# Performance work log

Measured on AMD Instinct MI355X. Metric: run time of the kernel, lower is better.

The kernel has to match this reference:

```python
import jax, jax.numpy as jnp
import numpy as np

B, N, V, F, H, O, NCONV = 4096, 64, 100, 128, 256, 1, 4
NEG_SLOPE = 0.01  # torch nn.LeakyReLU default


def leaky(x):
    return jnp.where(x >= 0, x, NEG_SLOPE * x)


def setup_inputs() -> dict:
    key = jax.random.key(0)
    ks = jax.random.split(key, 16)
    node_mat = jax.random.normal(ks[0], (B, N, V), dtype=jnp.float32)
    a = (jax.random.uniform(ks[1], (B, N, N)) < 0.15).astype(jnp.float32)
    adj_mat = jnp.maximum(a, jnp.swapaxes(a, 1, 2))
    s = 0.05
    params = dict(
        W_init=s * jax.random.normal(ks[2], (V, F), jnp.float32),
        b_init=jnp.zeros((F,), jnp.float32),
        W_conv=s * jax.random.normal(ks[3], (NCONV, F, F), jnp.float32),
        b_conv=jnp.zeros((NCONV, F), jnp.float32),
        W_fc0=s * jax.random.normal(ks[4], (F, H), jnp.float32),
        b_fc0=jnp.zeros((H,), jnp.float32),
        W_fc1=s * jax.random.normal(ks[5], (H, H), jnp.float32),
        b_fc1=jnp.zeros((H,), jnp.float32),
        W_out=s * jax.random.normal(ks[6], (H, O), jnp.float32),
        b_out=jnp.zeros((O,), jnp.float32),
    )
    return dict(node_mat=node_mat, adj_mat=adj_mat, **params)


def reference(node_mat, adj_mat, W_init, b_init, W_conv, b_conv,
              W_fc0, b_fc0, W_fc1, b_fc1, W_out, b_out):
    # init transform + LeakyReLU
    x = leaky(node_mat @ W_init + b_init)                      # [B, N, F]
    # degree-normalized adjacency: diag(1/deg) @ A == row-scale (exact same math
    # as the original eye-expand + double bmm, without the NxN diagonal matmul)
    deg = jnp.clip(adj_mat.sum(axis=-1, keepdims=True), 1.0, None)  # [B, N, 1]
    A_norm = adj_mat / deg                                     # [B, N, N]
    for i in range(W_conv.shape[0]):
        agg = jnp.einsum('bij,bjf->bif', A_norm, x)            # neighbor mean
        x = leaky(agg @ W_conv[i] + b_conv[i])
    # mean pooling over atoms
    g = x.mean(axis=1)                                         # [B, F]
    # fc head (dropout p=0 -> identity)
    h = leaky(g @ W_fc0 + b_fc0)
    h = leaky(h @ W_fc1 + b_fc1)
    return h @ W_out + b_out                                   # [B, O]
```

## Files before the change

kernel.cpp:

```cpp
#include <hip/hip_runtime.h>

#define NATOMS 64
#define VDIM 100
#define FDIM 128
#define HDIM 256
#define NCONV 4

typedef __bf16 bf16x8 __attribute__((ext_vector_type(8)));
typedef __bf16 bf16x4 __attribute__((ext_vector_type(4)));
typedef float f32x4 __attribute__((ext_vector_type(4)));

__device__ __forceinline__ float lrelu(float x) {
  return x >= 0.0f ? x : 0.01f * x;
}

__global__ void prep_weights(const float* __restrict__ Wi,
                             const float* __restrict__ Wc,
                             __bf16* __restrict__ WtI,
                             __bf16* __restrict__ WtC) {
  int idx = blockIdx.x * 256 + threadIdx.x;
  int e = idx & 7;
  int lane = (idx >> 3) & 63;
  int ks = (idx >> 9) & 3;
  int n16 = (idx >> 11) & 7;
  int l = idx >> 14;
  int n = n16 * 16 + (lane & 15);
  int k = ks * 32 + (lane >> 4) * 8 + e;
  if (l == 0) {
    WtI[idx] = (__bf16)(k < VDIM ? Wi[k * FDIM + n] : 0.0f);
  } else {
    WtC[(l - 1) * 16384 + (idx & 16383)] =
        (__bf16)Wc[(l - 1) * FDIM * FDIM + k * FDIM + n];
  }
}

template <bool PRODUCE_FRAG>
__device__ __forceinline__ void conv_step(
    const __bf16* __restrict__ Wt, const float* __restrict__ bias,
    const __bf16* __restrict__ sRow, bf16x8 xfrag[2][2], float psum[2],
    const int w, const int lane) {
  const int lr = lane & 15;
  const int g = lane >> 4;
  const int k0 = g * 8;
  f32x4 acc[2][4];
#pragma unroll
  for (int ni = 0; ni < 2; ++ni)
#pragma unroll
    for (int mi = 0; mi < 4; ++mi) acc[ni][mi] = {0.f, 0.f, 0.f, 0.f};
#pragma unroll
  for (int ks = 0; ks < 4; ++ks) {
    bf16x8 bfrag[2], afrag[4];
#pragma unroll
    for (int ni = 0; ni < 2; ++ni)
      bfrag[ni] = *(const bf16x8*)&Wt[(((2 * w + ni) * 4 + ks) * 64 + lane) * 8];
#pragma unroll
    for (int mi = 0; mi < 4; ++mi) {
      int m = mi * 16 + lr;
      afrag[mi] = *(const bf16x8*)&sRow[m * 128 + ((ks * 32 + k0) ^ ((m & 7) << 3))];
    }
#pragma unroll
    for (int ni = 0; ni < 2; ++ni)
#pragma unroll
      for (int mi = 0; mi < 4; ++mi)
        acc[ni][mi] = __builtin_amdgcn_mfma_f32_16x16x32_bf16(
            afrag[mi], bfrag[ni], acc[ni][mi], 0, 0, 0);
  }
#pragma unroll
  for (int ni = 0; ni < 2; ++ni) {
    float bv = bias[(2 * w + ni) * 16 + lr];
    if constexpr (PRODUCE_FRAG) {
      uint2 d[4];
#pragma unroll
      for (int mi = 0; mi < 4; ++mi) {
        bf16x4 o;
#pragma unroll
        for (int j = 0; j < 4; ++j) o[j] = (__bf16)lrelu(acc[ni][mi][j] + bv);
        d[mi] = __builtin_bit_cast(uint2, o);
      }
#pragma unroll
      for (int ksp = 0; ksp < 2; ++ksp) {
        unsigned r[4];
#pragma unroll
        for (int q = 0; q < 4; ++q) {
          int src = (2 * (g & 1) + (q >> 1)) * 16 + lr;
          unsigned lo = (q & 1) ? d[2 * ksp].y : d[2 * ksp].x;
          unsigned hi = (q & 1) ? d[2 * ksp + 1].y : d[2 * ksp + 1].x;
          unsigned va = (unsigned)__shfl((int)lo, src);
          unsigned vb = (unsigned)__shfl((int)hi, src);
          r[q] = (g >> 1) ? vb : va;
        }
        xfrag[ni][ksp] =
            __builtin_bit_cast(bf16x8, make_uint4(r[0], r[1], r[2], r[3]));
      }
    } else {
      float s = 0.f;
#pragma unroll
      for (int mi = 0; mi < 4; ++mi)
#pragma unroll
        for (int j = 0; j < 4; ++j) s += lrelu(acc[ni][mi][j] + bv);
      psum[ni] = s;
    }
  }
}

__device__ __forceinline__ void agg_step(const __bf16* __restrict__ sAdj,
                                         const bf16x8 xfrag[2][2],
                                         __bf16* __restrict__ sRow,
                                         const float rdgv[4], const int w,
                                         const int lane) {
  const int lr = lane & 15;
  const int g = lane >> 4;
  const int k0 = g * 8;
  f32x4 acc[2][4];
#pragma unroll
  for (int mi = 0; mi < 2; ++mi)
#pragma unroll
    for (int ni = 0; ni < 4; ++ni) acc[mi][ni] = {0.f, 0.f, 0.f, 0.f};
#pragma unroll
  for (int ks = 0; ks < 2; ++ks) {
    bf16x8 bfrag[4];
#pragma unroll
    for (int ni = 0; ni < 4; ++ni) {
      int n = ni * 16 + lr;
      bfrag[ni] = *(const bf16x8*)&sAdj[n * 64 + ((ks * 32 + k0) ^ ((n & 7) << 3))];
    }
#pragma unroll
    for (int mi = 0; mi < 2; ++mi)
#pragma unroll
      for (int ni = 0; ni < 4; ++ni)
        acc[mi][ni] = __builtin_amdgcn_mfma_f32_16x16x32_bf16(
            xfrag[mi][ks], bfrag[ni], acc[mi][ni], 0, 0, 0);
  }
#pragma unroll
  for (int ni = 0; ni < 4; ++ni) {
    float rv = rdgv[ni];
    int a = ni * 16 + lr;
#pragma unroll
    for (int mi = 0; mi < 2; ++mi) {
      int f0r = (2 * w + mi) * 16 + g * 4;
      bf16x4 o;
#pragma unroll
      for (int j = 0; j < 4; ++j) o[j] = (__bf16)(acc[mi][ni][j] * rv);
      *(bf16x4*)&sRow[a * 128 + (f0r ^ ((a & 7) << 3))] = o;
    }
  }
}

__launch_bounds__(256, 4)
__global__ void gcn_mfma(const float* __restrict__ node,
                         const float* __restrict__ adj,
                         const __bf16* __restrict__ WtI,
                         const __bf16* __restrict__ WtC,
                         const float* __restrict__ b_init,
                         const float* __restrict__ b_conv,
                         float* __restrict__ g_out) {
  __shared__ __align__(16) __bf16 sRow[NATOMS * FDIM];
  __shared__ __align__(16) __bf16 sAdj[NATOMS * NATOMS];
  __shared__ float sRdg[NATOMS];

  const int b = blockIdx.x;
  const int t = threadIdx.x;
  const int lane = t & 63;
  const int w = t >> 6;

  {
    const float* adjB = adj + (size_t)b * NATOMS * NATOMS;
#pragma unroll
    for (int half = 0; half < 2; ++half) {
      int n = (t >> 3) + half * 32;
      int gi = t & 7;
      float4 a0 = *(const float4*)&adjB[n * 64 + gi * 8];
      float4 a1 = *(const float4*)&adjB[n * 64 + gi * 8 + 4];
      bf16x8 v;
      v[0] = (__bf16)a0.x; v[1] = (__bf16)a0.y; v[2] = (__bf16)a0.z; v[3] = (__bf16)a0.w;
      v[4] = (__bf16)a1.x; v[5] = (__bf16)a1.y; v[6] = (__bf16)a1.z; v[7] = (__bf16)a1.w;
      *(bf16x8*)&sAdj[n * 64 + ((gi * 8) ^ ((n & 7) << 3))] = v;
      float p = a0.x + a0.y + a0.z + a0.w + a1.x + a1.y + a1.z + a1.w;
      p += __shfl_xor(p, 1); p += __shfl_xor(p, 2); p += __shfl_xor(p, 4);
      if (gi == 0) sRdg[n] = 1.0f / fmaxf(p, 1.0f);
    }
  }
  {
    const float* nodeB = node + (size_t)b * NATOMS * VDIM;
#pragma unroll
    for (int u0 = 0; u0 < 4; ++u0) {
      int u = t + 256 * u0;
      int n = u >> 4, gi = u & 15, kk = gi * 8;
      bf16x8 v;
      if (kk + 8 <= VDIM) {
        float4 a0 = *(const float4*)&nodeB[n * VDIM + kk];
        float4 a1 = *(const float4*)&nodeB[n * VDIM + kk + 4];
        v[0] = (__bf16)a0.x; v[1] = (__bf16)a0.y; v[2] = (__bf16)a0.z; v[3] = (__bf16)a0.w;
        v[4] = (__bf16)a1.x; v[5] = (__bf16)a1.y; v[6] = (__bf16)a1.z; v[7] = (__bf16)a1.w;
      } else {
#pragma unroll
        for (int i = 0; i < 8; ++i)
          v[i] = (__bf16)((kk + i < VDIM) ? nodeB[n * VDIM + kk + i] : 0.0f);
      }
      *(bf16x8*)&sRow[n * 128 + (kk ^ ((n & 7) << 3))] = v;
    }
  }
  __syncthreads();

  float rdgv[4];
#pragma unroll
  for (int ni = 0; ni < 4; ++ni) rdgv[ni] = sRdg[ni * 16 + (lane & 15)];

  bf16x8 xfrag[2][2];
  float psum[2];

  conv_step<true>(WtI, b_init, sRow, xfrag, psum, w, lane);
  __syncthreads();

#pragma unroll
  for (int l = 0; l < NCONV; ++l) {
    agg_step(sAdj, xfrag, sRow, rdgv, w, lane);
    __syncthreads();
    if (l < NCONV - 1) {
      conv_step<true>(WtC + l * 16384, b_conv + l * FDIM, sRow, xfrag, psum, w, lane);
      __syncthreads();
    } else {
      conv_step<false>(WtC + l * 16384, b_conv + l * FDIM, sRow, xfrag, psum, w, lane);
    }
  }

#pragma unroll
  for (int ni = 0; ni < 2; ++ni) {
    float s = psum[ni];
    s += __shfl_xor(s, 16);
    s += __shfl_xor(s, 32);
    if (lane < 16)
      g_out[(size_t)b * FDIM + (2 * w + ni) * 16 + lane] = s * (1.0f / 64.0f);
  }
}

__launch_bounds__(256, 2)
__global__ void head_fc(const float* __restrict__ g,
                        const float* __restrict__ W_fc0, const float* __restrict__ b_fc0,
                        const float* __restrict__ W_fc1, const float* __restrict__ b_fc1,
                        const float* __restrict__ W_out, const float* __restrict__ b_out,
                        float* __restrict__ out) {
  __shared__ __align__(16) float sG[16 * FDIM];
  __shared__ float sH[16 * (HDIM + 1)];
  __shared__ float sRed[4 * 16];

  const int t = threadIdx.x;
  const int lane = t & 63;
  const int w = t >> 6;
  const int r0 = blockIdx.x * 16;

  {
    const float4* gs = (const float4*)(g + (size_t)r0 * FDIM);
    float4* gd = (float4*)sG;
#pragma unroll
    for (int u = 0; u < 2; ++u) gd[t + 256 * u] = gs[t + 256 * u];
  }
  __syncthreads();

  float acc[16];
  {
    float bv = b_fc0[t];
#pragma unroll
    for (int r = 0; r < 16; ++r) acc[r] = bv;
    for (int k = 0; k < FDIM; ++k) {
      float wv = W_fc0[k * HDIM + t];
#pragma unroll
      for (int r = 0; r < 16; ++r) acc[r] += sG[r * FDIM + k] * wv;
    }
#pragma unroll
    for (int r = 0; r < 16; ++r) sH[r * (HDIM + 1) + t] = lrelu(acc[r]);
  }
  __syncthreads();

  {
    float bv = b_fc1[t];
#pragma unroll
    for (int r = 0; r < 16; ++r) acc[r] = bv;
    for (int k = 0; k < HDIM; ++k) {
      float wv = W_fc1[k * HDIM + t];
#pragma unroll
      for (int r = 0; r < 16; ++r) acc[r] += sH[r * (HDIM + 1) + k] * wv;
    }
    float wo = W_out[t];
#pragma unroll
    for (int r = 0; r < 16; ++r) acc[r] = lrelu(acc[r]) * wo;
  }
#pragma unroll
  for (int r = 0; r < 16; ++r) {
    float v = acc[r];
    v += __shfl_down(v, 32); v += __shfl_down(v, 16); v += __shfl_down(v, 8);
    v += __shfl_down(v, 4);  v += __shfl_down(v, 2);  v += __shfl_down(v, 1);
    if (lane == 0) sRed[w * 16 + r] = v;
  }
  __syncthreads();
  if (t < 16)
    out[r0 + t] = sRed[t] + sRed[16 + t] + sRed[32 + t] + sRed[48 + t] + b_out[0];
}

extern "C" void kernel_launch(void* const* d_in, const int* in_sizes, int n_in,
                              void* d_out, int out_size, void* d_ws, size_t ws_size,
                              hipStream_t stream) {
  (void)in_sizes; (void)n_in; (void)ws_size; (void)out_size;
  const float* node   = (const float*)d_in[0];
  const float* adj    = (const float*)d_in[1];
  const float* W_init = (const float*)d_in[2];
  const float* b_init = (const float*)d_in[3];
  const float* W_conv = (const float*)d_in[4];
  const float* b_conv = (const float*)d_in[5];
  const float* W_fc0  = (const float*)d_in[6];
  const float* b_fc0  = (const float*)d_in[7];
  const float* W_fc1  = (const float*)d_in[8];
  const float* b_fc1  = (const float*)d_in[9];
  const float* W_out  = (const float*)d_in[10];
  const float* b_out  = (const float*)d_in[11];
  float* out = (float*)d_out;

  __bf16* WtI = (__bf16*)d_ws;
  __bf16* WtC = WtI + 16384;
  float* g = (float*)((char*)d_ws + 160 * 1024);

  prep_weights<<<320, 256, 0, stream>>>(W_init, W_conv, WtI, WtC);
  gcn_mfma<<<4096, 256, 0, stream>>>(node, adj, WtI, WtC, b_init, b_conv, g);
  head_fc<<<256, 256, 0, stream>>>(g, W_fc0, b_fc0, W_fc1, b_fc1, W_out, b_out, out);
}
```

Before: 142.2 us.

## Double-buffer node features in LDS and keep adjacency fragments in registers

Node features now alternate between two LDS buffers across layers. This drops the barrier after each convolution step. The adjacency MFMA B-fragments are loaded from LDS once into registers and reused by all four aggregation steps, and the adjacency staging area is aliased onto the second feature buffer. The cost is more LDS per block (32KB instead of 24KB) and about 32 extra VGPRs, which could add register pressure or spills under the 4-blocks-per-CU launch bound.

Result: slower. 147.5 us (+3.7%).

```diff
diff --git a/kernel.cpp b/kernel.cpp
--- a/kernel.cpp
+++ b/kernel.cpp
@@ -37,7 +37,7 @@
 template <bool PRODUCE_FRAG>
 __device__ __forceinline__ void conv_step(
     const __bf16* __restrict__ Wt, const float* __restrict__ bias,
-    const __bf16* __restrict__ sRow, bf16x8 xfrag[2][2], float psum[2],
+    const __bf16* __restrict__ bufIn, bf16x8 xfrag[2][2], float psum[2],
     const int w, const int lane) {
   const int lr = lane & 15;
   const int g = lane >> 4;
@@ -56,7 +56,7 @@
 #pragma unroll
     for (int mi = 0; mi < 4; ++mi) {
       int m = mi * 16 + lr;
-      afrag[mi] = *(const bf16x8*)&sRow[m * 128 + ((ks * 32 + k0) ^ ((m & 7) << 3))];
+      afrag[mi] = *(const bf16x8*)&bufIn[m * 128 + ((ks * 32 + k0) ^ ((m & 7) << 3))];
     }
 #pragma unroll
     for (int ni = 0; ni < 2; ++ni)
@@ -103,34 +103,26 @@
   }
 }
 
-__device__ __forceinline__ void agg_step(const __bf16* __restrict__ sAdj,
+__device__ __forceinline__ void agg_step(const bf16x8 abfrag[4][2],
                                          const bf16x8 xfrag[2][2],
-                                         __bf16* __restrict__ sRow,
+                                         __bf16* __restrict__ bufOut,
                                          const float rdgv[4], const int w,
                                          const int lane) {
   const int lr = lane & 15;
   const int g = lane >> 4;
-  const int k0 = g * 8;
   f32x4 acc[2][4];
 #pragma unroll
   for (int mi = 0; mi < 2; ++mi)
 #pragma unroll
     for (int ni = 0; ni < 4; ++ni) acc[mi][ni] = {0.f, 0.f, 0.f, 0.f};
 #pragma unroll
-  for (int ks = 0; ks < 2; ++ks) {
-    bf16x8 bfrag[4];
-#pragma unroll
-    for (int ni = 0; ni < 4; ++ni) {
-      int n = ni * 16 + lr;
-      bfrag[ni] = *(const bf16x8*)&sAdj[n * 64 + ((ks * 32 + k0) ^ ((n & 7) << 3))];
-    }
+  for (int ks = 0; ks < 2; ++ks)
 #pragma unroll
     for (int mi = 0; mi < 2; ++mi)
 #pragma unroll
       for (int ni = 0; ni < 4; ++ni)
         acc[mi][ni] = __builtin_amdgcn_mfma_f32_16x16x32_bf16(
-            xfrag[mi][ks], bfrag[ni], acc[mi][ni], 0, 0, 0);
-  }
+            xfrag[mi][ks], abfrag[ni][ks], acc[mi][ni], 0, 0, 0);
 #pragma unroll
   for (int ni = 0; ni < 4; ++ni) {
     float rv = rdgv[ni];
@@ -141,7 +133,7 @@
       bf16x4 o;
 #pragma unroll
       for (int j = 0; j < 4; ++j) o[j] = (__bf16)(acc[mi][ni][j] * rv);
-      *(bf16x4*)&sRow[a * 128 + (f0r ^ ((a & 7) << 3))] = o;
+      *(bf16x4*)&bufOut[a * 128 + (f0r ^ ((a & 7) << 3))] = o;
     }
   }
 }
@@ -154,14 +146,18 @@
                          const float* __restrict__ b_init,
                          const float* __restrict__ b_conv,
                          float* __restrict__ g_out) {
-  __shared__ __align__(16) __bf16 sRow[NATOMS * FDIM];
-  __shared__ __align__(16) __bf16 sAdj[NATOMS * NATOMS];
+  __shared__ __align__(16) __bf16 sBuf[2 * NATOMS * FDIM];
   __shared__ float sRdg[NATOMS];
+  __bf16* buf0 = sBuf;
+  __bf16* buf1 = sBuf + NATOMS * FDIM;
+  __bf16* sAdj = buf1;
 
   const int b = blockIdx.x;
   const int t = threadIdx.x;
   const int lane = t & 63;
   const int w = t >> 6;
+  const int lr = lane & 15;
+  const int k0 = (lane >> 4) * 8;
 
   {
     const float* adjB = adj + (size_t)b * NATOMS * NATOMS;
@@ -197,31 +193,38 @@
         for (int i = 0; i < 8; ++i)
           v[i] = (__bf16)((kk + i < VDIM) ? nodeB[n * VDIM + kk + i] : 0.0f);
       }
-      *(bf16x8*)&sRow[n * 128 + (kk ^ ((n & 7) << 3))] = v;
-    }
-  }
-  __syncthreads();
-
+      *(bf16x8*)&buf0[n * 128 + (kk ^ ((n & 7) << 3))] = v;
+    }
+  }
+  __syncthreads();
+
+  bf16x8 abfrag[4][2];
+#pragma unroll
+  for (int ni = 0; ni < 4; ++ni)
+#pragma unroll
+    for (int ks = 0; ks < 2; ++ks) {
+      int n = ni * 16 + lr;
+      abfrag[ni][ks] = *(const bf16x8*)&sAdj[n * 64 + ((ks * 32 + k0) ^ ((n & 7) << 3))];
+    }
   float rdgv[4];
 #pragma unroll
-  for (int ni = 0; ni < 4; ++ni) rdgv[ni] = sRdg[ni * 16 + (lane & 15)];
+  for (int ni = 0; ni < 4; ++ni) rdgv[ni] = sRdg[ni * 16 + lr];
 
   bf16x8 xfrag[2][2];
   float psum[2];
 
-  conv_step<true>(WtI, b_init, sRow, xfrag, psum, w, lane);
+  conv_step<true>(WtI, b_init, buf0, xfrag, psum, w, lane);
   __syncthreads();
 
 #pragma unroll
   for (int l = 0; l < NCONV; ++l) {
-    agg_step(sAdj, xfrag, sRow, rdgv, w, lane);
+    __bf16* bufW = sBuf + ((l + 1) & 1) * NATOMS * FDIM;
+    agg_step(abfrag, xfrag, bufW, rdgv, w, lane);
     __syncthreads();
-    if (l < NCONV - 1) {
-      conv_step<true>(WtC + l * 16384, b_conv + l * FDIM, sRow, xfrag, psum, w, lane);
-      __syncthreads();
-    } else {
-      conv_step<false>(WtC + l * 16384, b_conv + l * FDIM, sRow, xfrag, psum, w, lane);
-    }
+    if (l < NCONV - 1)
+      conv_step<true>(WtC + l * 16384, b_conv + l * FDIM, bufW, xfrag, psum, w, lane);
+    else
+      conv_step<false>(WtC + l * 16384, b_conv + l * FDIM, bufW, xfrag, psum, w, lane);
   }
 
 #pragma unroll
```
